# Optimization experiments

Hardware: AMD Instinct MI355X
Metric: run time of the kernel (lower is better)

## Reference

```python
import jax, jax.numpy as jnp
import numpy as np

D = 64               # embed_dim
DM = 2 * D           # d_model = 128
DI = 2 * DM          # support-encoder inner = 256
HID = 2 * DM         # LSTMCell hidden = 256
B = 128              # query batch
NN = 200             # max neighbors (hard-coded in docstring)
FEW = 5              # support set size
NUM_ENTS = 50000
NUM_RELS = 500
STEPS = 4            # process_steps
LN_EPS = 1e-3


def setup_inputs() -> dict:
    key = jax.random.key(0)
    ks = jax.random.split(key, 16)
    s = 0.05
    return {
        "q_left_conn":  jax.random.randint(ks[0], (B, NN, 2), 0, NUM_RELS),
        "q_right_conn": jax.random.randint(ks[1], (B, NN, 2), 0, NUM_RELS),
        "s_left_conn":  jax.random.randint(ks[2], (FEW, NN, 2), 0, NUM_RELS),
        "s_right_conn": jax.random.randint(ks[3], (FEW, NN, 2), 0, NUM_RELS),
        "q_left_deg":  jnp.floor(jax.random.uniform(ks[4], (B,)) * 199.0) + 1.0,
        "q_right_deg": jnp.floor(jax.random.uniform(ks[5], (B,)) * 199.0) + 1.0,
        "s_left_deg":  jnp.floor(jax.random.uniform(ks[6], (FEW,)) * 199.0) + 1.0,
        "s_right_deg": jnp.floor(jax.random.uniform(ks[7], (FEW,)) * 199.0) + 1.0,
        "ent_emb": jax.random.normal(ks[8], (NUM_ENTS + 1, D)) * s,
        "rel_mat": jax.random.normal(ks[9], (NUM_RELS + 1, D * D)) * s,
        "gcn_w":  jax.random.normal(ks[10], (D, D)) * s,
        "gcn_wb": jnp.zeros((D,)),
        "gcn_b":  jnp.zeros((D,)),
        "se_w1": jax.random.normal(ks[11], (DM, DI)) * s,
        "se_b1": jnp.zeros((DI,)),
        "se_w2": jax.random.normal(ks[12], (DI, DM)) * s,
        "se_b2": jnp.zeros((DM,)),
        "ln_g": jnp.ones((DM,)),
        "ln_b": jnp.zeros((DM,)),
        "lstm_wih": jax.random.normal(ks[13], (DM, 4 * HID)) * s,
        "lstm_whh": jax.random.normal(ks[14], (HID, 4 * HID)) * s,
        "lstm_bih": jnp.zeros((4 * HID,)),
        "lstm_bhh": jnp.zeros((4 * HID,)),
    }


def _neighbor_encoder(conn, deg, ent_emb, rel_mat, gcn_w, gcn_wb, gcn_b):
    # conn: (b, n, 2) int -> (relation, entity)
    rel_idx = conn[:, :, 0]
    ent_idx = conn[:, :, 1]
    R = rel_mat[rel_idx].reshape(rel_idx.shape[0], rel_idx.shape[1], D, D)  # (b, n, D, D)
    e = ent_emb[ent_idx]                                                    # (b, n, D)
    msg = jnp.einsum('bnij,bnj->bni', R, e)       # per-neighbor RESCAL bmm
    out = msg @ gcn_w + gcn_wb + gcn_b            # gcn_w linear + gcn_b
    out = out.sum(axis=1) / deg[:, None]          # sum-reduce over neighbors, normalize
    return jnp.tanh(out)                          # (b, D)


def _support_encoder(x, w1, b1, w2, b2, g, b):
    # FFN + residual + LayerNormalization (torch std is unbiased, eps=1e-3)
    h = jax.nn.relu(x @ w1 + b1) @ w2 + b2 + x
    mu = h.mean(axis=-1, keepdims=True)
    sigma = jnp.std(h, axis=-1, keepdims=True, ddof=1)
    return (h - mu) / (sigma + LN_EPS) * g + b


def _query_encoder(support, query, wih, whh, bih, bhh):
    # LSTM "process" block: input is always `query`, gate order i,f,g,o (torch LSTMCell)
    bsz = query.shape[0]
    h_r = jnp.zeros((bsz, HID), query.dtype)
    c = jnp.zeros((bsz, HID), query.dtype)
    x_proj = query @ wih + bih + bhh              # input projection is step-invariant
    h = query
    for _ in range(STEPS):
        gates = x_proj + h_r @ whh
        i, f, g, o = jnp.split(gates, 4, axis=-1)
        c = jax.nn.sigmoid(f) * c + jax.nn.sigmoid(i) * jnp.tanh(g)
        h_r_ = jax.nn.sigmoid(o) * jnp.tanh(c)
        h = query + h_r_[:, :DM]
        attn = jax.nn.softmax(h @ support.T, axis=1)
        r = attn @ support
        h_r = jnp.concatenate([h, r], axis=1)
    return h


def reference(q_left_conn, q_right_conn, s_left_conn, s_right_conn,
              q_left_deg, q_right_deg, s_left_deg, s_right_deg,
              ent_emb, rel_mat, gcn_w, gcn_wb, gcn_b,
              se_w1, se_b1, se_w2, se_b2, ln_g, ln_b,
              lstm_wih, lstm_whh, lstm_bih, lstm_bhh):
    # dropout layers are identity in eval mode
    ne = lambda conn, deg: _neighbor_encoder(conn, deg, ent_emb, rel_mat, gcn_w, gcn_wb, gcn_b)
    query = jnp.concatenate([ne(q_left_conn, q_left_deg), ne(q_right_conn, q_right_deg)], axis=-1)      # (B, 2D)
    support = jnp.concatenate([ne(s_left_conn, s_left_deg), ne(s_right_conn, s_right_deg)], axis=-1)    # (FEW, 2D)
    support_g = _support_encoder(support, se_w1, se_b1, se_w2, se_b2, ln_g, ln_b)
    query_g = _support_encoder(query, se_w1, se_b1, se_w2, se_b2, ln_g, ln_b)
    query_f = _query_encoder(support_g, query_g, lstm_wih, lstm_whh, lstm_bih, lstm_bhh)
    return query_f @ support_g.T                  # matching_scores (B, FEW)
```

## Files before the change

kernel.cpp:

```cpp
#include <hip/hip_runtime.h>
#include <math.h>

#define NREL 500
#define CAP  256
#define NEDGE 53200

__device__ __forceinline__ float sigm(float x) { return 1.0f / (1.0f + __expf(-x)); }
__device__ __forceinline__ unsigned bf16_rne(float x) {
    unsigned b = __float_as_uint(x);
    return (b + 0x7fffu + ((b >> 16) & 1u)) >> 16;
}

#define OFF_COUNTS 0
#define OFF_LIST   512
#define OFF_WHHP   256512
#define OFF_WIHP   322048
#define OFF_QG     354816
#define OFF_SG     371200
#define OFF_STAGE  371840

__global__ __launch_bounds__(512) void k_build(
    const int* __restrict__ qlc, const int* __restrict__ qrc,
    const int* __restrict__ slc, const int* __restrict__ srcn,
    const float* __restrict__ whh, const float* __restrict__ wih,
    float* __restrict__ ws)
{
    const int idx = blockIdx.x * 512 + threadIdx.x;
    if (idx < NEDGE) {
        unsigned* counts = (unsigned*)(ws + OFF_COUNTS);
        int2* list2 = (int2*)(ws + OFF_LIST);
        const int e = idx;
        const int* cp; int i, dest;
        if (e < 25600)      { cp = qlc;  i = e;         dest = i / 200; }
        else if (e < 51200) { cp = qrc;  i = e - 25600; dest = 128 + i / 200; }
        else if (e < 52200) { cp = slc;  i = e - 51200; dest = 256 + i / 200; }
        else                { cp = srcn; i = e - 52200; dest = 261 + i / 200; }
        const int rel = cp[2 * i];
        const int ent = cp[2 * i + 1];
        const unsigned ret = atomicAdd(&counts[rel], 1u);
        const int slot = (int)(ret & (CAP - 1));
        const int meta = 0x50000000 | (e << 9) | dest;
        list2[rel * CAP + slot] = make_int2(ent, meta);
    } else if (idx < NEDGE + 98304) {
        unsigned* whhp = (unsigned*)(ws + OFF_WHHP);
        unsigned* wihp = (unsigned*)(ws + OFF_WIHP);
        const int p = idx - NEDGE;
        if (p < 65536) {
            const int v = p & 511, jp = p >> 9;
            const int u = ((v >> 7) << 8) + (v & 127);
            whhp[jp * 512 + v] = bf16_rne(whh[(2 * jp) * 1024 + u]) |
                                 (bf16_rne(whh[(2 * jp + 1) * 1024 + u]) << 16);
        } else {
            const int g2 = p - 65536;
            const int v = g2 & 511, jp = g2 >> 9;
            const int u = ((v >> 7) << 8) + (v & 127);
            wihp[jp * 512 + v] = bf16_rne(wih[(2 * jp) * 1024 + u]) |
                                 (bf16_rne(wih[(2 * jp + 1) * 1024 + u]) << 16);
        }
    }
}

__global__ __launch_bounds__(256, 2) void k_gather(
    const float* __restrict__ rel_mat, const float* __restrict__ ent_emb,
    float* __restrict__ ws)
{
    const int r    = blockIdx.x;
    const int tid  = threadIdx.x;
    const int wave = tid >> 6, lane = tid & 63;
    const int2* list2 = (const int2*)(ws + OFF_LIST) + r * CAP;
    unsigned* stage_u = (unsigned*)(ws + OFF_STAGE);

    __shared__ int2 lst[CAP];
    __shared__ int  lcnt;
    if (tid == 0) lcnt = 0;

    float Rr[64];
    {
        const float4* Rp = reinterpret_cast<const float4*>(rel_mat + (size_t)r * 4096 + lane * 64);
#pragma unroll
        for (int q = 0; q < 16; ++q) {
            const float4 v = Rp[q];
            Rr[4 * q + 0] = v.x; Rr[4 * q + 1] = v.y;
            Rr[4 * q + 2] = v.z; Rr[4 * q + 3] = v.w;
        }
    }
    __syncthreads();

    {
        const int2 en = list2[tid];
        const int meta = en.y;
        const int e = (meta >> 9) & 0xffff, dest = meta & 511;
        const bool ok = ((meta >> 28) & 0xf) == 0x5 && e < NEDGE && dest < 266 &&
                        en.x >= 0 && en.x <= 50000;
        if (ok) {
            const int s = atomicAdd(&lcnt, 1);
            lst[s] = en;
        }
    }
    __syncthreads();
    const int cnt = lcnt;

    for (int m = wave; m < cnt; m += 4) {
        const int2 ed = lst[m];
        const int ent = __builtin_amdgcn_readfirstlane(ed.x);
        const int e   = __builtin_amdgcn_readfirstlane((ed.y >> 9) & 0xffff);
        const float4* ep = reinterpret_cast<const float4*>(ent_emb + (size_t)ent * 64);
        float a0 = 0.f, a1 = 0.f;
#pragma unroll
        for (int q = 0; q < 8; ++q) {
            const float4 e0 = ep[2 * q];
            const float4 e1 = ep[2 * q + 1];
            a0 = fmaf(Rr[8 * q + 0], e0.x, a0);
            a0 = fmaf(Rr[8 * q + 1], e0.y, a0);
            a0 = fmaf(Rr[8 * q + 2], e0.z, a0);
            a0 = fmaf(Rr[8 * q + 3], e0.w, a0);
            a1 = fmaf(Rr[8 * q + 4], e1.x, a1);
            a1 = fmaf(Rr[8 * q + 5], e1.y, a1);
            a1 = fmaf(Rr[8 * q + 6], e1.z, a1);
            a1 = fmaf(Rr[8 * q + 7], e1.w, a1);
        }
        const float acc = a0 + a1;
        const float par = __shfl_xor(acc, 1);
        if (!(lane & 1)) {
            const unsigned u = bf16_rne(acc) | (bf16_rne(par) << 16);
            stage_u[(size_t)e * 32 + (lane >> 1)] = u;
        }
    }
}

__global__ __launch_bounds__(256) void k_post(
    const float* __restrict__ gcn_w, const float* __restrict__ gcn_wb,
    const float* __restrict__ gcn_b,
    const float* __restrict__ qld, const float* __restrict__ qrd,
    const float* __restrict__ sld, const float* __restrict__ srd,
    const float* __restrict__ w1, const float* __restrict__ b1,
    const float* __restrict__ w2, const float* __restrict__ b2,
    const float* __restrict__ lng, const float* __restrict__ lnb,
    float* __restrict__ ws)
{
    const int blk = blockIdx.x, t = threadIdx.x;
    const unsigned* stage_u = (const unsigned*)(ws + OFF_STAGE);

    __shared__ float mm[128];
    __shared__ float degs[2];
    __shared__ float x[128];
    __shared__ float h1[256];
    __shared__ float hh[128];
    __shared__ float red[8];

    if (t < 128) mm[t] = 0.f;
    if (t < 2) {
        const float* dp;
        if (blk < 128) dp = t ? qrd + blk : qld + blk;
        else           dp = t ? srd + (blk - 128) : sld + (blk - 128);
        degs[t] = dp[0];
    }
    __syncthreads();

    {
        const int half = t >> 7, rr = t & 127, cp = rr >> 2, q = rr & 3;
        int e0;
        if (blk < 128) e0 = half ? 25600 + blk * 200 : blk * 200;
        else { const int f = blk - 128; e0 = half ? 52200 + f * 200 : 51200 + f * 200; }
        const unsigned* sp = stage_u + (size_t)(e0 + q * 50) * 32 + cp;
        float slo = 0.f, shi = 0.f;
#pragma unroll 10
        for (int n = 0; n < 50; ++n) {
            const unsigned u = sp[n * 32];
            slo += __uint_as_float(u << 16);
            shi += __uint_as_float(u & 0xffff0000u);
        }
        atomicAdd(&mm[half * 64 + 2 * cp], slo);
        atomicAdd(&mm[half * 64 + 2 * cp + 1], shi);
    }
    __syncthreads();

    if (t < 128) {
        const int col = t & 63, base = t & 64;
        float s = 0.f;
#pragma unroll 8
        for (int j = 0; j < 64; ++j) s = fmaf(mm[base + j], gcn_w[j * 64 + col], s);
        s += 200.f * (gcn_wb[col] + gcn_b[col]);
        x[t] = tanhf(s / degs[t >> 6]);
    }
    __syncthreads();

    {
        float s = b1[t];
#pragma unroll 8
        for (int j = 0; j < 128; ++j) s = fmaf(x[j], w1[j * 256 + t], s);
        h1[t] = fmaxf(s, 0.f);
    }
    __syncthreads();
    if (t < 128) {
        float s = b2[t] + x[t];
#pragma unroll 8
        for (int k = 0; k < 256; ++k) s = fmaf(h1[k], w2[k * 128 + t], s);
        hh[t] = s;
    }
    __syncthreads();

    float v = (t < 128) ? hh[t] : 0.f;
#pragma unroll
    for (int m = 32; m >= 1; m >>= 1) v += __shfl_xor(v, m);
    if ((t & 63) == 0) red[t >> 6] = v;
    __syncthreads();
    const float mu = (red[0] + red[1]) * (1.f / 128.f);
    float d = (t < 128) ? (hh[t] - mu) : 0.f;
    float v2 = d * d;
#pragma unroll
    for (int m = 32; m >= 1; m >>= 1) v2 += __shfl_xor(v2, m);
    if ((t & 63) == 0) red[4 + (t >> 6)] = v2;
    __syncthreads();
    const float var = (red[4] + red[5]) * (1.f / 127.f);
    const float rs = 1.f / (sqrtf(var) + 0.001f);
    if (t < 128) {
        float* xout = (blk < 128) ? ws + OFF_QG + blk * 128 : ws + OFF_SG + (blk - 128) * 128;
        xout[t] = (hh[t] - mu) * rs * lng[t] + lnb[t];
    }
}

__global__ __launch_bounds__(512) void k_lstm(
    const float* __restrict__ bih, const float* __restrict__ bhh,
    float* __restrict__ ws, float* __restrict__ outp)
{
    const int t = threadIdx.x;
    const int b = blockIdx.x;
    const unsigned* whhp = (const unsigned*)(ws + OFF_WHHP);
    const unsigned* wihp = (const unsigned*)(ws + OFF_WIHP);

    __shared__ float sgf[5 * 128];
    __shared__ float qg[128];
    __shared__ float hr[256];
    __shared__ float gbuf[512];
    __shared__ float redw[2][5];

    for (int i = t; i < 640; i += 512) sgf[i] = (ws + OFF_SG)[i];
    if (t < 128) qg[t] = (ws + OFF_QG)[(size_t)b * 128 + t];
    if (t < 256) hr[t] = 0.f;

    const int u = ((t >> 7) << 8) + (t & 127);
    float xp = bih[u] + bhh[u];
    __syncthreads();

    const float2* qg2 = (const float2*)qg;
    const float2* hr2 = (const float2*)hr;

#pragma unroll 8
    for (int jp = 0; jp < 64; ++jp) {
        const unsigned w = wihp[jp * 512 + t];
        const float2 q = qg2[jp];
        xp = fmaf(__uint_as_float(w << 16), q.x,
             fmaf(__uint_as_float(w & 0xffff0000u), q.y, xp));
    }

    float c = 0.f;
    const int tp = t & 127;

    for (int step = 0; step < 4; ++step) {
        float g0 = xp, g1 = 0.f, g2 = 0.f, g3 = 0.f;
#pragma unroll 4
        for (int jp = 0; jp < 128; jp += 4) {
            const unsigned w0 = whhp[(jp + 0) * 512 + t];
            const unsigned w1 = whhp[(jp + 1) * 512 + t];
            const unsigned w2 = whhp[(jp + 2) * 512 + t];
            const unsigned w3 = whhp[(jp + 3) * 512 + t];
            const float2 h0 = hr2[jp + 0], h1 = hr2[jp + 1];
            const float2 h2 = hr2[jp + 2], h3 = hr2[jp + 3];
            g0 = fmaf(__uint_as_float(w0 << 16), h0.x, fmaf(__uint_as_float(w0 & 0xffff0000u), h0.y, g0));
            g1 = fmaf(__uint_as_float(w1 << 16), h1.x, fmaf(__uint_as_float(w1 & 0xffff0000u), h1.y, g1));
            g2 = fmaf(__uint_as_float(w2 << 16), h2.x, fmaf(__uint_as_float(w2 & 0xffff0000u), h2.y, g2));
            g3 = fmaf(__uint_as_float(w3 << 16), h3.x, fmaf(__uint_as_float(w3 & 0xffff0000u), h3.y, g3));
        }
        gbuf[t] = (g0 + g1) + (g2 + g3);
        __syncthreads();

        float hv = 0.f;
        if (t < 128) {
            const float iv = sigm(gbuf[tp]);
            const float fv = sigm(gbuf[128 + tp]);
            const float gv = tanhf(gbuf[256 + tp]);
            const float ov = sigm(gbuf[384 + tp]);
            c = fv * c + iv * gv;
            hv = qg[tp] + ov * tanhf(c);
            hr[tp] = hv;
        }

        float p0 = 0, p1 = 0, p2 = 0, p3 = 0, p4 = 0;
        if (t < 128) {
            p0 = hv * sgf[0 * 128 + tp];
            p1 = hv * sgf[1 * 128 + tp];
            p2 = hv * sgf[2 * 128 + tp];
            p3 = hv * sgf[3 * 128 + tp];
            p4 = hv * sgf[4 * 128 + tp];
#pragma unroll
            for (int m = 32; m >= 1; m >>= 1) {
                p0 += __shfl_xor(p0, m);
                p1 += __shfl_xor(p1, m);
                p2 += __shfl_xor(p2, m);
                p3 += __shfl_xor(p3, m);
                p4 += __shfl_xor(p4, m);
            }
            if ((t & 63) == 0) {
                const int w = t >> 6;
                redw[w][0] = p0; redw[w][1] = p1; redw[w][2] = p2;
                redw[w][3] = p3; redw[w][4] = p4;
            }
        }
        __syncthreads();

        const float d0 = redw[0][0] + redw[1][0];
        const float d1 = redw[0][1] + redw[1][1];
        const float d2 = redw[0][2] + redw[1][2];
        const float d3 = redw[0][3] + redw[1][3];
        const float d4 = redw[0][4] + redw[1][4];

        if (step == 3) {
            if (t == 0) {
                float* o = outp + (size_t)b * 5;
                o[0] = d0; o[1] = d1; o[2] = d2; o[3] = d3; o[4] = d4;
            }
        }
        if (t < 128) {
            const float mx = fmaxf(fmaxf(fmaxf(d0, d1), fmaxf(d2, d3)), d4);
            const float e0 = __expf(d0 - mx), e1 = __expf(d1 - mx), e2 = __expf(d2 - mx),
                        e3 = __expf(d3 - mx), e4 = __expf(d4 - mx);
            const float inv = 1.f / (e0 + e1 + e2 + e3 + e4);
            hr[128 + tp] = (e0 * sgf[0 * 128 + tp] + e1 * sgf[1 * 128 + tp] +
                            e2 * sgf[2 * 128 + tp] + e3 * sgf[3 * 128 + tp] +
                            e4 * sgf[4 * 128 + tp]) * inv;
        }
        __syncthreads();
    }
}

extern "C" void kernel_launch(void* const* d_in, const int* in_sizes, int n_in,
                              void* d_out, int out_size, void* d_ws, size_t ws_size,
                              hipStream_t stream) {
    const int*   qlc = (const int*)d_in[0];
    const int*   qrc = (const int*)d_in[1];
    const int*   slc = (const int*)d_in[2];
    const int*   srcn= (const int*)d_in[3];
    const float* qld = (const float*)d_in[4];
    const float* qrd = (const float*)d_in[5];
    const float* sld = (const float*)d_in[6];
    const float* srd = (const float*)d_in[7];
    const float* ent = (const float*)d_in[8];
    const float* rel = (const float*)d_in[9];
    const float* gw  = (const float*)d_in[10];
    const float* gwb = (const float*)d_in[11];
    const float* gb  = (const float*)d_in[12];
    const float* w1  = (const float*)d_in[13];
    const float* b1  = (const float*)d_in[14];
    const float* w2  = (const float*)d_in[15];
    const float* b2  = (const float*)d_in[16];
    const float* lng = (const float*)d_in[17];
    const float* lnb = (const float*)d_in[18];
    const float* wih = (const float*)d_in[19];
    const float* whh = (const float*)d_in[20];
    const float* bih = (const float*)d_in[21];
    const float* bhh = (const float*)d_in[22];

    float* ws   = (float*)d_ws;
    float* outp = (float*)d_out;

    hipLaunchKernelGGL(k_build,  dim3(296), dim3(512), 0, stream,
                       qlc, qrc, slc, srcn, whh, wih, ws);
    hipLaunchKernelGGL(k_gather, dim3(NREL), dim3(256), 0, stream, rel, ent, ws);
    hipLaunchKernelGGL(k_post,   dim3(133), dim3(256), 0, stream,
                       gw, gwb, gb, qld, qrd, sld, srd,
                       w1, b1, w2, b2, lng, lnb, ws);
    hipLaunchKernelGGL(k_lstm,   dim3(128), dim3(512), 0, stream, bih, bhh, ws, outp);
}
```

Measured before the change: 194.3 us.

## Fuse edge bucketing and weight packing into gather kernel via per-block edge scan

```diff
diff --git a/kernel.cpp b/kernel.cpp
--- a/kernel.cpp
+++ b/kernel.cpp
@@ -11,63 +11,22 @@
     return (b + 0x7fffu + ((b >> 16) & 1u)) >> 16;
 }
 
-#define OFF_COUNTS 0
-#define OFF_LIST   512
-#define OFF_WHHP   256512
-#define OFF_WIHP   322048
-#define OFF_QG     354816
-#define OFF_SG     371200
-#define OFF_STAGE  371840
-
-__global__ __launch_bounds__(512) void k_build(
+#define OFF_WHHP   0
+#define OFF_WIHP   65536
+#define OFF_QG     98304
+#define OFF_SG     114688
+#define OFF_STAGE  115328
+
+__global__ __launch_bounds__(256, 2) void k_gather(
     const int* __restrict__ qlc, const int* __restrict__ qrc,
     const int* __restrict__ slc, const int* __restrict__ srcn,
+    const float* __restrict__ rel_mat, const float* __restrict__ ent_emb,
     const float* __restrict__ whh, const float* __restrict__ wih,
-    float* __restrict__ ws)
-{
-    const int idx = blockIdx.x * 512 + threadIdx.x;
-    if (idx < NEDGE) {
-        unsigned* counts = (unsigned*)(ws + OFF_COUNTS);
-        int2* list2 = (int2*)(ws + OFF_LIST);
-        const int e = idx;
-        const int* cp; int i, dest;
-        if (e < 25600)      { cp = qlc;  i = e;         dest = i / 200; }
-        else if (e < 51200) { cp = qrc;  i = e - 25600; dest = 128 + i / 200; }
-        else if (e < 52200) { cp = slc;  i = e - 51200; dest = 256 + i / 200; }
-        else                { cp = srcn; i = e - 52200; dest = 261 + i / 200; }
-        const int rel = cp[2 * i];
-        const int ent = cp[2 * i + 1];
-        const unsigned ret = atomicAdd(&counts[rel], 1u);
-        const int slot = (int)(ret & (CAP - 1));
-        const int meta = 0x50000000 | (e << 9) | dest;
-        list2[rel * CAP + slot] = make_int2(ent, meta);
-    } else if (idx < NEDGE + 98304) {
-        unsigned* whhp = (unsigned*)(ws + OFF_WHHP);
-        unsigned* wihp = (unsigned*)(ws + OFF_WIHP);
-        const int p = idx - NEDGE;
-        if (p < 65536) {
-            const int v = p & 511, jp = p >> 9;
-            const int u = ((v >> 7) << 8) + (v & 127);
-            whhp[jp * 512 + v] = bf16_rne(whh[(2 * jp) * 1024 + u]) |
-                                 (bf16_rne(whh[(2 * jp + 1) * 1024 + u]) << 16);
-        } else {
-            const int g2 = p - 65536;
-            const int v = g2 & 511, jp = g2 >> 9;
-            const int u = ((v >> 7) << 8) + (v & 127);
-            wihp[jp * 512 + v] = bf16_rne(wih[(2 * jp) * 1024 + u]) |
-                                 (bf16_rne(wih[(2 * jp + 1) * 1024 + u]) << 16);
-        }
-    }
-}
-
-__global__ __launch_bounds__(256, 2) void k_gather(
-    const float* __restrict__ rel_mat, const float* __restrict__ ent_emb,
     float* __restrict__ ws)
 {
     const int r    = blockIdx.x;
     const int tid  = threadIdx.x;
     const int wave = tid >> 6, lane = tid & 63;
-    const int2* list2 = (const int2*)(ws + OFF_LIST) + r * CAP;
     unsigned* stage_u = (unsigned*)(ws + OFF_STAGE);
 
     __shared__ int2 lst[CAP];
@@ -86,24 +45,25 @@
     }
     __syncthreads();
 
-    {
-        const int2 en = list2[tid];
-        const int meta = en.y;
-        const int e = (meta >> 9) & 0xffff, dest = meta & 511;
-        const bool ok = ((meta >> 28) & 0xf) == 0x5 && e < NEDGE && dest < 266 &&
-                        en.x >= 0 && en.x <= 50000;
-        if (ok) {
-            const int s = atomicAdd(&lcnt, 1);
-            lst[s] = en;
-        }
-    }
-    __syncthreads();
-    const int cnt = lcnt;
+    for (int e = tid; e < NEDGE; e += 256) {
+        const int2* cp; int i;
+        if (e < 25600)      { cp = (const int2*)qlc;  i = e; }
+        else if (e < 51200) { cp = (const int2*)qrc;  i = e - 25600; }
+        else if (e < 52200) { cp = (const int2*)slc;  i = e - 51200; }
+        else                { cp = (const int2*)srcn; i = e - 52200; }
+        const int2 ce = cp[i];
+        if (ce.x == r) {
+            const int slot = atomicAdd(&lcnt, 1);
+            if (slot < CAP) lst[slot] = make_int2(ce.y, e);
+        }
+    }
+    __syncthreads();
+    const int cnt = min(lcnt, CAP);
 
     for (int m = wave; m < cnt; m += 4) {
         const int2 ed = lst[m];
         const int ent = __builtin_amdgcn_readfirstlane(ed.x);
-        const int e   = __builtin_amdgcn_readfirstlane((ed.y >> 9) & 0xffff);
+        const int e   = __builtin_amdgcn_readfirstlane(ed.y);
         const float4* ep = reinterpret_cast<const float4*>(ent_emb + (size_t)ent * 64);
         float a0 = 0.f, a1 = 0.f;
 #pragma unroll
@@ -122,8 +82,27 @@
         const float acc = a0 + a1;
         const float par = __shfl_xor(acc, 1);
         if (!(lane & 1)) {
-            const unsigned u = bf16_rne(acc) | (bf16_rne(par) << 16);
-            stage_u[(size_t)e * 32 + (lane >> 1)] = u;
+            stage_u[(size_t)e * 32 + (lane >> 1)] = bf16_rne(acc) | (bf16_rne(par) << 16);
+        }
+    }
+
+    {
+        const int idx = r * 256 + tid;
+        if (idx < 98304) {
+            unsigned* whhp = (unsigned*)(ws + OFF_WHHP);
+            unsigned* wihp = (unsigned*)(ws + OFF_WIHP);
+            if (idx < 65536) {
+                const int v = idx & 511, jp = idx >> 9;
+                const int u = ((v >> 7) << 8) + (v & 127);
+                whhp[jp * 512 + v] = bf16_rne(whh[(2 * jp) * 1024 + u]) |
+                                     (bf16_rne(whh[(2 * jp + 1) * 1024 + u]) << 16);
+            } else {
+                const int g2 = idx - 65536;
+                const int v = g2 & 511, jp = g2 >> 9;
+                const int u = ((v >> 7) << 8) + (v & 127);
+                wihp[jp * 512 + v] = bf16_rne(wih[(2 * jp) * 1024 + u]) |
+                                     (bf16_rne(wih[(2 * jp + 1) * 1024 + u]) << 16);
+            }
         }
     }
 }
@@ -141,37 +120,45 @@
     const int blk = blockIdx.x, t = threadIdx.x;
     const unsigned* stage_u = (const unsigned*)(ws + OFF_STAGE);
 
-    __shared__ float mm[128];
-    __shared__ float degs[2];
-    __shared__ float x[128];
-    __shared__ float h1[256];
-    __shared__ float hh[128];
-    __shared__ float red[8];
-
-    if (t < 128) mm[t] = 0.f;
+    __shared__ float2 mmw[4][32];
+    __shared__ float  mm[128];
+    __shared__ float  degs[2];
+    __shared__ float  x[128];
+    __shared__ float  h1[256];
+    __shared__ float  hh[128];
+    __shared__ float  red[8];
+
     if (t < 2) {
         const float* dp;
         if (blk < 128) dp = t ? qrd + blk : qld + blk;
         else           dp = t ? srd + (blk - 128) : sld + (blk - 128);
         degs[t] = dp[0];
     }
-    __syncthreads();
 
     {
-        const int half = t >> 7, rr = t & 127, cp = rr >> 2, q = rr & 3;
+        const int w = t >> 6, lane = t & 63;
+        const int half = w >> 1, wl = w & 1;
+        const int c = lane & 31, rp = lane >> 5;
         int e0;
         if (blk < 128) e0 = half ? 25600 + blk * 200 : blk * 200;
         else { const int f = blk - 128; e0 = half ? 52200 + f * 200 : 51200 + f * 200; }
-        const unsigned* sp = stage_u + (size_t)(e0 + q * 50) * 32 + cp;
+        const unsigned* sp = stage_u + (size_t)e0 * 32 + (wl * 2 + rp) * 32 + c;
         float slo = 0.f, shi = 0.f;
 #pragma unroll 10
-        for (int n = 0; n < 50; ++n) {
-            const unsigned u = sp[n * 32];
+        for (int it = 0; it < 50; ++it) {
+            const unsigned u = sp[it * 128];
             slo += __uint_as_float(u << 16);
             shi += __uint_as_float(u & 0xffff0000u);
         }
-        atomicAdd(&mm[half * 64 + 2 * cp], slo);
-        atomicAdd(&mm[half * 64 + 2 * cp + 1], shi);
+        slo += __shfl_xor(slo, 32);
+        shi += __shfl_xor(shi, 32);
+        if (rp == 0) mmw[w][c] = make_float2(slo, shi);
+    }
+    __syncthreads();
+    if (t < 64) {
+        const int half = t >> 5, c = t & 31;
+        const float2 a = mmw[half * 2][c], b = mmw[half * 2 + 1][c];
+        ((float2*)mm)[half * 32 + c] = make_float2(a.x + b.x, a.y + b.y);
     }
     __syncthreads();
 
@@ -364,9 +351,8 @@
     float* ws   = (float*)d_ws;
     float* outp = (float*)d_out;
 
-    hipLaunchKernelGGL(k_build,  dim3(296), dim3(512), 0, stream,
-                       qlc, qrc, slc, srcn, whh, wih, ws);
-    hipLaunchKernelGGL(k_gather, dim3(NREL), dim3(256), 0, stream, rel, ent, ws);
+    hipLaunchKernelGGL(k_gather, dim3(NREL), dim3(256), 0, stream,
+                       qlc, qrc, slc, srcn, rel, ent, whh, wih, ws);
     hipLaunchKernelGGL(k_post,   dim3(133), dim3(256), 0, stream,
                        gw, gwb, gb, qld, qrd, sld, srd,
                        w1, b1, w2, b2, lng, lnb, ws);
```

New measurement: 240.2 us. 1.24x slower.
